# Performance work log

Hardware: AMD Instinct MI355X
Metric: run time of the kernel (lower is better)

Reference implementation:

```python
import jax, jax.numpy as jnp
import numpy as np

N_WAY = 5
NKPTS = 17
EMBED = 512
N_SUPPORT = 25  # 5-way 5-shot
N_QUERY = 65536


def setup_inputs() -> dict:
    key = jax.random.key(0)
    ks = jax.random.split(key, 12)
    def lin(k, fan_in, fan_out):
        return jax.random.normal(k, (fan_in, fan_out), jnp.float32) / np.float32(np.sqrt(fan_in))
    return {
        'support_features': jax.random.normal(ks[0], (1, N_SUPPORT, EMBED), jnp.float32),
        'support_keypoints': jax.random.uniform(ks[1], (N_SUPPORT, NKPTS, 2), jnp.float32),
        'query_features': jax.random.normal(ks[2], (N_QUERY, EMBED), jnp.float32),
        'image_coords': jax.random.uniform(ks[3], (N_QUERY, 2), jnp.float32) * 512.0,
        'W1': lin(ks[4], EMBED, EMBED), 'b1': jnp.zeros((EMBED,), jnp.float32),
        'W2': lin(ks[5], EMBED, EMBED), 'b2': jnp.zeros((EMBED,), jnp.float32),
        'Wo1': lin(ks[6], EMBED, EMBED // 2), 'bo1': jnp.zeros((EMBED // 2,), jnp.float32),
        'Wo2': lin(ks[7], EMBED // 2, 2), 'bo2': jnp.zeros((2,), jnp.float32),
        'Wc1': lin(ks[8], EMBED, EMBED // 2), 'bc1': jnp.zeros((EMBED // 2,), jnp.float32),
        'Wc2': lin(ks[9], EMBED // 2, 1), 'bc2': jnp.zeros((1,), jnp.float32),
        'temperature': jnp.float32(1.0),
    }


def reference(support_features, support_keypoints, query_features, image_coords,
              W1, b1, W2, b2, Wo1, bo1, Wo2, bo2, Wc1, bc1, Wc2, bc2, temperature):
    eps = 1e-8
    nkpts = support_keypoints.shape[1]
    n_query = query_features.shape[0]
    D = query_features.shape[-1]

    # --- compute_prototypes (batch_size == 1; per-kpt prototype identical by construction) ---
    sf = support_features.reshape(-1, D)                      # [Ns, D]
    h = jnp.maximum(sf @ W1 + b1, 0.0) @ W2 + b2              # prototype_net MLP
    n_per = h.shape[0] // N_WAY
    proto_way = h.reshape(N_WAY, n_per, D).mean(axis=1)       # [n_way, D]
    prototypes = jnp.broadcast_to(proto_way[:, None, :], (N_WAY, nkpts, D))

    # --- compute_distances: 1 - cosine_sim, scaled by temperature ---
    qn = jnp.linalg.norm(query_features, axis=-1)             # [Nq]
    pn = jnp.linalg.norm(proto_way, axis=-1)                  # [n_way]
    sim = (query_features @ proto_way.T) / jnp.maximum(qn[:, None] * pn[None, :], eps)
    dist_way = (1.0 - sim) / temperature                      # [Nq, n_way]
    distances = jnp.broadcast_to(dist_way[:, :, None], (n_query, N_WAY, nkpts))

    # --- predict_keypoints ---
    # avg over kpts is a no-op (identical per kpt); argmin over ways
    class_predictions = jnp.argmin(dist_way, axis=1)          # [Nq] int
    # softmax over a single scalar == 1.0, so keypoints == offset broadcast over kpts
    offset = jnp.maximum(query_features @ Wo1 + bo1, 0.0) @ Wo2 + bo2   # [Nq, 2]
    conf = jax.nn.sigmoid(jnp.maximum(query_features @ Wc1 + bc1, 0.0) @ Wc2 + bc2)  # [Nq, 1]
    keypoints = jnp.broadcast_to(offset[:, None, :], (n_query, nkpts, 2))
    keypoints = jax.nn.sigmoid(keypoints) * image_coords[:, None, :]    # image_coords provided
    confidence = jnp.broadcast_to(conf, (n_query, nkpts))

    return keypoints, confidence, distances, class_predictions, prototypes
```

## Files before the change

kernel.cpp:

```cpp
#include <hip/hip_runtime.h>
#include <hip/hip_bf16.h>

#define NQ 65536
#define DIM 512
#define HID 256
#define NWAY 5
#define NKPTS 17

typedef short bf16x8 __attribute__((ext_vector_type(8)));
typedef float f32x4 __attribute__((ext_vector_type(4)));
typedef _Float16 half8 __attribute__((ext_vector_type(8)));

static __device__ __forceinline__ unsigned short f2bf(float f) {
    unsigned int x = __float_as_uint(f);
    unsigned int r = (x + 0x7fffu + ((x >> 16) & 1u)) >> 16;
    return (unsigned short)r;
}

static __device__ __forceinline__ void async16(void* l, const void* g) {
    __builtin_amdgcn_global_load_lds(
        (const __attribute__((address_space(1))) unsigned int*)g,
        (__attribute__((address_space(3))) unsigned int*)l, 16, 0, 0);
}

__global__ __launch_bounds__(256) void k_sup(const float* __restrict__ sf,
                                             const float* __restrict__ W1, const float* __restrict__ b1,
                                             float* __restrict__ ws_h1) {
    __shared__ float sfl[512];
    __shared__ float red[4][64];
    int bx = blockIdx.x;
    int s = bx >> 3, cb = bx & 7;
    int t = threadIdx.x;
    if (t < 128) ((float4*)sfl)[t] = ((const float4*)(sf + s * DIM))[t];
    __syncthreads();
    int c = cb * 64 + (t & 63);
    int qd = t >> 6;
    const float* Wp = W1 + (size_t)qd * 128 * DIM + c;
    float acc = 0.0f;
    #pragma unroll 4
    for (int kk = 0; kk < 128; kk++)
        acc += sfl[qd * 128 + kk] * Wp[(size_t)kk * DIM];
    red[qd][t & 63] = acc;
    __syncthreads();
    if (t < 64) {
        float h = red[0][t] + red[1][t] + red[2][t] + red[3][t] + b1[cb * 64 + t];
        ws_h1[s * DIM + cb * 64 + t] = fmaxf(h, 0.0f);
    }
}

__global__ __launch_bounds__(256) void k_mid2(const float* __restrict__ ws_h1,
                                              const float* __restrict__ W2, const float* __restrict__ b2,
                                              const float* __restrict__ Wo1, const float* __restrict__ Wc1,
                                              float* __restrict__ ws_proto, unsigned short* __restrict__ wb) {
    int bx = blockIdx.x;
    int t = threadIdx.x;
    if (bx < 40) {
        __shared__ float ml[512];
        __shared__ float red[4][64];
        int w = bx >> 3, cb = bx & 7;
        for (int i = t; i < 512; i += 256) {
            float sum = 0.0f;
            #pragma unroll
            for (int s5 = 0; s5 < 5; s5++) sum += ws_h1[(w * 5 + s5) * DIM + i];
            ml[i] = sum * 0.2f;
        }
        __syncthreads();
        int c = cb * 64 + (t & 63);
        int qd = t >> 6;
        const float* Wp = W2 + (size_t)qd * 128 * DIM + c;
        float acc = 0.0f;
        #pragma unroll 4
        for (int kk = 0; kk < 128; kk++)
            acc += ml[qd * 128 + kk] * Wp[(size_t)kk * DIM];
        red[qd][t & 63] = acc;
        __syncthreads();
        if (t < 64)
            ws_proto[w * DIM + cb * 64 + t] =
                red[0][t] + red[1][t] + red[2][t] + red[3][t] + b2[cb * 64 + t];
    } else {
        __shared__ unsigned short T[64][72];
        int tb = bx - 40;
        const float* src = (tb < 32) ? Wo1 : Wc1;
        int cofs = (tb < 32) ? 0 : 256;
        int tt = tb & 31;
        int kt = tt >> 2;
        int ct = tt & 3;
        int i = t >> 2;
        int qd = t & 3;
        const float* rp = src + (size_t)(kt * 64 + i) * HID + ct * 64 + qd * 16;
        #pragma unroll
        for (int v = 0; v < 4; v++) {
            float4 x = *(const float4*)(rp + v * 4);
            T[qd * 16 + v * 4 + 0][i] = f2bf(x.x);
            T[qd * 16 + v * 4 + 1][i] = f2bf(x.y);
            T[qd * 16 + v * 4 + 2][i] = f2bf(x.z);
            T[qd * 16 + v * 4 + 3][i] = f2bf(x.w);
        }
        __syncthreads();
        int j = t >> 2;
        int part = t & 3;
        uint4 o0 = *(const uint4*)&T[j][part * 16];
        uint4 o1 = *(const uint4*)&T[j][part * 16 + 8];
        unsigned short* dst = wb + (size_t)(cofs + ct * 64 + j) * DIM + kt * 64 + part * 16;
        *(uint4*)dst = o0;
        *(uint4*)(dst + 8) = o1;
    }
}

__global__ __launch_bounds__(512) void k_fused3(const float* __restrict__ qf,
                                                const unsigned short* __restrict__ wb,
                                                const float* __restrict__ ws_proto,
                                                const float* __restrict__ temp_p,
                                                const float* __restrict__ bo1, const float* __restrict__ Wo2,
                                                const float* __restrict__ bo2,
                                                const float* __restrict__ bc1, const float* __restrict__ Wc2,
                                                const float* __restrict__ bc2,
                                                const float* __restrict__ ic,
                                                float* __restrict__ out_kp, float* __restrict__ out_conf,
                                                float* __restrict__ out_dist, float* __restrict__ out_class,
                                                float* __restrict__ out_proto) {
    __shared__ __align__(16) char smem[127520];
    char* Abase = smem;
    char* Bbase = smem + 16384;
    float* s_proto = (float*)(smem + 114688);
    float* dlds = (float*)(smem + 124928);
    float* pn_lds = (float*)(smem + 127488);
    _Float16* hl = (_Float16*)smem;
    float* redf = (float*)(smem + 67584);

    int mb = blockIdx.x;
    int t = threadIdx.x;
    int wv = t >> 6, lane = t & 63;
    int wr = wv >> 2, wc = wv & 3;
    int r = lane & 15, hq = lane >> 4;

    for (int i = t; i < NWAY * DIM; i += 512) s_proto[i] = ws_proto[i];
    if (mb < NWAY * NKPTS && t < 128) {
        f32x4 v = *(const f32x4*)(ws_proto + (mb / NKPTS) * DIM + t * 4);
        *(f32x4*)(out_proto + (size_t)mb * DIM + t * 4) = v;
    }
    float invt = 1.0f / temp_p[0];
    __syncthreads();

    if (wv < NWAY) {
        f32x4 a = *(const f32x4*)(s_proto + wv * DIM + lane * 8);
        f32x4 b = *(const f32x4*)(s_proto + wv * DIM + lane * 8 + 4);
        float ss = a[0]*a[0] + a[1]*a[1] + a[2]*a[2] + a[3]*a[3]
                 + b[0]*b[0] + b[1]*b[1] + b[2]*b[2] + b[3]*b[3];
        #pragma unroll
        for (int off = 32; off > 0; off >>= 1) ss += __shfl_xor(ss, off, 64);
        if (lane == 0) pn_lds[wv] = sqrtf(ss);
    }

    int am = t >> 2, akc = t & 3;
    const float* Ag = qf + ((size_t)mb * 128 + am) * DIM + akc * 8;
    int awoff = am * 64 + ((akc ^ (am & 3)) * 16);
    int srow = lane >> 2;
    int sg = (lane & 3) ^ (srow & 3);
    const unsigned short* Bg = wb + ((size_t)wv * 64 + srow) * DIM + sg * 8;

    f32x4 acc[4][8];
    #pragma unroll
    for (int i2 = 0; i2 < 4; i2++)
        #pragma unroll
        for (int j2 = 0; j2 < 8; j2++) { f32x4 z = {0.0f, 0.0f, 0.0f, 0.0f}; acc[i2][j2] = z; }
    float ds[NWAY] = {0, 0, 0, 0, 0};
    float qq = 0.0f;

    float4 aW0 = *(const float4*)(Ag);
    float4 aW1 = *(const float4*)(Ag + 4);
    float4 aN0 = *(const float4*)(Ag + 32);
    float4 aN1 = *(const float4*)(Ag + 36);
    #pragma unroll
    for (int i = 0; i < 4; i++)
        async16(Bbase + (wv * 4 + i) * 1024, Bg + (size_t)i * 16 * DIM);
    #pragma unroll
    for (int i = 0; i < 4; i++)
        async16(Bbase + 32768 + (wv * 4 + i) * 1024, Bg + (size_t)i * 16 * DIM + 32);

    {
        unsigned int p0 = f2bf(aW0.x) | ((unsigned int)f2bf(aW0.y) << 16);
        unsigned int p1 = f2bf(aW0.z) | ((unsigned int)f2bf(aW0.w) << 16);
        unsigned int p2 = f2bf(aW1.x) | ((unsigned int)f2bf(aW1.y) << 16);
        unsigned int p3 = f2bf(aW1.z) | ((unsigned int)f2bf(aW1.w) << 16);
        *(uint4*)(Abase + awoff) = make_uint4(p0, p1, p2, p3);
        float av[8] = {aW0.x, aW0.y, aW0.z, aW0.w, aW1.x, aW1.y, aW1.z, aW1.w};
        int kb = akc * 8;
        #pragma unroll
        for (int w = 0; w < NWAY; w++) {
            f32x4 pv0 = *(const f32x4*)(s_proto + w * DIM + kb);
            f32x4 pv1 = *(const f32x4*)(s_proto + w * DIM + kb + 4);
            ds[w] += av[0] * pv0[0] + av[1] * pv0[1] + av[2] * pv0[2] + av[3] * pv0[3]
                   + av[4] * pv1[0] + av[5] * pv1[1] + av[6] * pv1[2] + av[7] * pv1[3];
        }
        #pragma unroll
        for (int j = 0; j < 8; j++) qq += av[j] * av[j];
    }
    aW0 = aN0; aW1 = aN1;

    asm volatile("s_waitcnt lgkmcnt(0) vmcnt(4)" ::: "memory");
    __builtin_amdgcn_s_barrier();
    __builtin_amdgcn_sched_barrier(0);

    #pragma unroll 2
    for (int it = 0; it < 16; it++) {
        int apar = it & 1;
        int bpar = it % 3;
        float4 aL0, aL1;
        if (it < 14) {
            int ko = (it + 2) * 32;
            aL0 = *(const float4*)(Ag + ko);
            aL1 = *(const float4*)(Ag + ko + 4);
            int bp2 = (it + 2) % 3;
            #pragma unroll
            for (int i = 0; i < 4; i++)
                async16(Bbase + bp2 * 32768 + (wv * 4 + i) * 1024,
                        Bg + (size_t)i * 16 * DIM + ko);
        }
        if (it < 15) {
            unsigned int p0 = f2bf(aW0.x) | ((unsigned int)f2bf(aW0.y) << 16);
            unsigned int p1 = f2bf(aW0.z) | ((unsigned int)f2bf(aW0.w) << 16);
            unsigned int p2 = f2bf(aW1.x) | ((unsigned int)f2bf(aW1.y) << 16);
            unsigned int p3 = f2bf(aW1.z) | ((unsigned int)f2bf(aW1.w) << 16);
            *(uint4*)(Abase + (apar ^ 1) * 8192 + awoff) = make_uint4(p0, p1, p2, p3);
            float av[8] = {aW0.x, aW0.y, aW0.z, aW0.w, aW1.x, aW1.y, aW1.z, aW1.w};
            int kb = (it + 1) * 32 + akc * 8;
            #pragma unroll
            for (int w = 0; w < NWAY; w++) {
                f32x4 pv0 = *(const f32x4*)(s_proto + w * DIM + kb);
                f32x4 pv1 = *(const f32x4*)(s_proto + w * DIM + kb + 4);
                ds[w] += av[0] * pv0[0] + av[1] * pv0[1] + av[2] * pv0[2] + av[3] * pv0[3]
                       + av[4] * pv1[0] + av[5] * pv1[1] + av[6] * pv1[2] + av[7] * pv1[3];
            }
            #pragma unroll
            for (int j = 0; j < 8; j++) qq += av[j] * av[j];
        }
        const unsigned short* Ap = (const unsigned short*)(Abase + apar * 8192);
        const unsigned short* Bp = (const unsigned short*)(Bbase + bpar * 32768);
        int sl = (hq ^ (r & 3)) * 8;
        bf16x8 af[4], bfr[8];
        #pragma unroll
        for (int mt = 0; mt < 4; mt++)
            af[mt] = *(const bf16x8*)(Ap + (wr * 64 + mt * 16 + r) * 32 + sl);
        #pragma unroll
        for (int nt = 0; nt < 8; nt++)
            bfr[nt] = *(const bf16x8*)(Bp + (wc * 128 + nt * 16 + r) * 32 + sl);
        #pragma unroll
        for (int mt = 0; mt < 4; mt++)
            #pragma unroll
            for (int nt = 0; nt < 8; nt++)
                acc[mt][nt] = __builtin_amdgcn_mfma_f32_16x16x32_bf16(af[mt], bfr[nt], acc[mt][nt], 0, 0, 0);
        if (it < 15) {
            if (it < 14) { asm volatile("s_waitcnt lgkmcnt(0) vmcnt(6)" ::: "memory"); }
            else         { asm volatile("s_waitcnt lgkmcnt(0) vmcnt(0)" ::: "memory"); }
            __builtin_amdgcn_s_barrier();
            __builtin_amdgcn_sched_barrier(0);
        }
        if (it < 14) { aW0 = aL0; aW1 = aL1; }
    }
    __syncthreads();

    if (wc < 2) {
        #pragma unroll
        for (int nt = 0; nt < 8; nt++) {
            int cl = wc * 128 + nt * 16 + r;
            float bv = bo1[cl];
            #pragma unroll
            for (int mt = 0; mt < 4; mt++)
                #pragma unroll
                for (int rg = 0; rg < 4; rg++) {
                    int ml = wr * 64 + mt * 16 + hq * 4 + rg;
                    hl[ml * 264 + cl] = (_Float16)fmaxf(acc[mt][nt][rg] + bv, 0.0f);
                }
        }
    }
    __syncthreads();

    #pragma unroll
    for (int off = 1; off <= 2; off <<= 1) {
        #pragma unroll
        for (int w = 0; w < NWAY; w++) ds[w] += __shfl_xor(ds[w], off, 64);
        qq += __shfl_xor(qq, off, 64);
    }
    if (akc == 0) {
        float qn = sqrtf(qq);
        float mv = 1e30f; int ami = 0;
        #pragma unroll
        for (int w = 0; w < NWAY; w++) {
            float den = fmaxf(qn * pn_lds[w], 1e-8f);
            float d = (1.0f - ds[w] / den) * invt;
            dlds[am * 5 + w] = d;
            if (d < mv) { mv = d; ami = w; }
        }
        out_class[mb * 128 + am] = (float)ami;
    }
    {
        int q = t & 127, qt = t >> 7;
        float ox = 0.0f, oy = 0.0f;
        #pragma unroll 2
        for (int j0 = 0; j0 < 64; j0 += 8) {
            half8 hv = *(const half8*)(hl + q * 264 + qt * 64 + j0);
            #pragma unroll
            for (int j = 0; j < 8; j++) {
                float2 w2 = *(const float2*)(Wo2 + (qt * 64 + j0 + j) * 2);
                float hf = (float)hv[j];
                ox += hf * w2.x;
                oy += hf * w2.y;
            }
        }
        redf[(qt * 128 + q) * 2] = ox;
        redf[(qt * 128 + q) * 2 + 1] = oy;
    }
    __syncthreads();

    if (t < 128) {
        float sx = bo2[0], sy = bo2[1];
        #pragma unroll
        for (int k2 = 0; k2 < 4; k2++) {
            sx += redf[(k2 * 128 + t) * 2];
            sy += redf[(k2 * 128 + t) * 2 + 1];
        }
        size_t Q = (size_t)mb * 128 + t;
        float2 icv = *(const float2*)(ic + Q * 2);
        float gx = icv.x / (1.0f + __expf(-sx));
        float gy = icv.y / (1.0f + __expf(-sy));
        float2 g2 = make_float2(gx, gy);
        float2* dst = (float2*)(out_kp + Q * 34);
        #pragma unroll
        for (int k2 = 0; k2 < 17; k2++) dst[k2] = g2;
    }
    if (wc >= 2) {
        #pragma unroll
        for (int nt = 0; nt < 8; nt++) {
            int cl = (wc - 2) * 128 + nt * 16 + r;
            float bv = bc1[cl];
            #pragma unroll
            for (int mt = 0; mt < 4; mt++)
                #pragma unroll
                for (int rg = 0; rg < 4; rg++) {
                    int ml = wr * 64 + mt * 16 + hq * 4 + rg;
                    hl[ml * 264 + cl] = (_Float16)fmaxf(acc[mt][nt][rg] + bv, 0.0f);
                }
        }
    }
    for (int i = t; i < 128 * NWAY * NKPTS; i += 512) {
        int q2 = i / (NWAY * NKPTS);
        int rem = i - q2 * (NWAY * NKPTS);
        out_dist[(size_t)(mb * 128 + q2) * (NWAY * NKPTS) + rem] = dlds[q2 * 5 + rem / NKPTS];
    }
    __syncthreads();

    {
        int q = t & 127, qt = t >> 7;
        float cs = 0.0f;
        #pragma unroll 2
        for (int j0 = 0; j0 < 64; j0 += 8) {
            half8 hv = *(const half8*)(hl + q * 264 + qt * 64 + j0);
            #pragma unroll
            for (int j = 0; j < 8; j++)
                cs += (float)hv[j] * Wc2[qt * 64 + j0 + j];
        }
        redf[qt * 128 + q] = cs;
    }
    __syncthreads();
    if (t < 128) {
        float s = bc2[0] + redf[t] + redf[128 + t] + redf[256 + t] + redf[384 + t];
        float sg2 = 1.0f / (1.0f + __expf(-s));
        size_t Q = (size_t)mb * 128 + t;
        float* dst = out_conf + Q * 17;
        #pragma unroll
        for (int k2 = 0; k2 < 17; k2++) dst[k2] = sg2;
    }
}

extern "C" void kernel_launch(void* const* d_in, const int* in_sizes, int n_in,
                              void* d_out, int out_size, void* d_ws, size_t ws_size,
                              hipStream_t stream) {
    const float* sf = (const float*)d_in[0];
    const float* qf = (const float*)d_in[2];
    const float* ic = (const float*)d_in[3];
    const float* W1 = (const float*)d_in[4];
    const float* b1 = (const float*)d_in[5];
    const float* W2 = (const float*)d_in[6];
    const float* b2 = (const float*)d_in[7];
    const float* Wo1 = (const float*)d_in[8];
    const float* bo1 = (const float*)d_in[9];
    const float* Wo2 = (const float*)d_in[10];
    const float* bo2 = (const float*)d_in[11];
    const float* Wc1 = (const float*)d_in[12];
    const float* bc1 = (const float*)d_in[13];
    const float* Wc2 = (const float*)d_in[14];
    const float* bc2 = (const float*)d_in[15];
    const float* temp = (const float*)d_in[16];

    float* out = (float*)d_out;
    float* out_kp = out;
    float* out_conf = out + 2228224;
    float* out_dist = out + 3342336;
    float* out_class = out + 8912896;
    float* out_proto = out + 8978432;

    char* ws = (char*)d_ws;
    float* ws_h1 = (float*)ws;
    float* ws_proto = (float*)(ws + 51200);
    unsigned short* ws_wb = (unsigned short*)(ws + 65536);

    hipLaunchKernelGGL(k_sup, dim3(200), dim3(256), 0, stream, sf, W1, b1, ws_h1);
    hipLaunchKernelGGL(k_mid2, dim3(104), dim3(256), 0, stream, ws_h1, W2, b2, Wo1, Wc1, ws_proto, ws_wb);
    hipLaunchKernelGGL(k_fused3, dim3(512), dim3(512), 0, stream, qf, ws_wb, ws_proto, temp,
                       bo1, Wo2, bo2, bc1, Wc2, bc2, ic, out_kp, out_conf,
                       out_dist, out_class, out_proto);
}
```

Before: 318.2 us.

## Split fused query kernel into separate distance kernel and N-split GEMM kernel

```diff
diff --git a/kernel.cpp b/kernel.cpp
--- a/kernel.cpp
+++ b/kernel.cpp
@@ -107,195 +107,208 @@
     }
 }
 
-__global__ __launch_bounds__(512) void k_fused3(const float* __restrict__ qf,
-                                                const unsigned short* __restrict__ wb,
-                                                const float* __restrict__ ws_proto,
-                                                const float* __restrict__ temp_p,
-                                                const float* __restrict__ bo1, const float* __restrict__ Wo2,
-                                                const float* __restrict__ bo2,
-                                                const float* __restrict__ bc1, const float* __restrict__ Wc2,
-                                                const float* __restrict__ bc2,
-                                                const float* __restrict__ ic,
-                                                float* __restrict__ out_kp, float* __restrict__ out_conf,
-                                                float* __restrict__ out_dist, float* __restrict__ out_class,
-                                                float* __restrict__ out_proto) {
-    __shared__ __align__(16) char smem[127520];
-    char* Abase = smem;
-    char* Bbase = smem + 16384;
-    float* s_proto = (float*)(smem + 114688);
-    float* dlds = (float*)(smem + 124928);
-    float* pn_lds = (float*)(smem + 127488);
+__global__ __launch_bounds__(256) void k_dist(const float* __restrict__ qf,
+                                              const float* __restrict__ ws_proto,
+                                              const float* __restrict__ temp_p,
+                                              float* __restrict__ out_dist, float* __restrict__ out_class,
+                                              float* __restrict__ out_proto) {
+    __shared__ float pn_lds[8];
+    __shared__ float dlds[64 * NWAY];
+    int bx = blockIdx.x, t = threadIdx.x;
+    int wv = t >> 6, lane = t & 63;
+
+    if (bx < NWAY * NKPTS && t < 128) {
+        f32x4 v = *(const f32x4*)(ws_proto + (bx / NKPTS) * DIM + t * 4);
+        *(f32x4*)(out_proto + (size_t)bx * DIM + t * 4) = v;
+    }
+    for (int w = wv; w < NWAY; w += 4) {
+        f32x4 a = *(const f32x4*)(ws_proto + w * DIM + lane * 8);
+        f32x4 b = *(const f32x4*)(ws_proto + w * DIM + lane * 8 + 4);
+        float ss = a[0]*a[0] + a[1]*a[1] + a[2]*a[2] + a[3]*a[3]
+                 + b[0]*b[0] + b[1]*b[1] + b[2]*b[2] + b[3]*b[3];
+        #pragma unroll
+        for (int off = 32; off > 0; off >>= 1) ss += __shfl_xor(ss, off, 64);
+        if (lane == 0) pn_lds[w] = sqrtf(ss);
+    }
+    float invt = 1.0f / temp_p[0];
+    __syncthreads();
+
+    int q = bx * 64 + wv * 16 + (lane & 15);
+    int kq = (lane >> 4) * 128;
+    const float* qp = qf + (size_t)q * DIM + kq;
+    const float* pp = ws_proto + kq;
+
+    float ds[NWAY] = {0, 0, 0, 0, 0};
+    float qq = 0.0f;
+    #pragma unroll 4
+    for (int c = 0; c < 16; c++) {
+        f32x4 v0 = *(const f32x4*)(qp + c * 8);
+        f32x4 v1 = *(const f32x4*)(qp + c * 8 + 4);
+        qq += v0[0]*v0[0] + v0[1]*v0[1] + v0[2]*v0[2] + v0[3]*v0[3]
+            + v1[0]*v1[0] + v1[1]*v1[1] + v1[2]*v1[2] + v1[3]*v1[3];
+        #pragma unroll
+        for (int w = 0; w < NWAY; w++) {
+            f32x4 p0 = *(const f32x4*)(pp + w * DIM + c * 8);
+            f32x4 p1 = *(const f32x4*)(pp + w * DIM + c * 8 + 4);
+            ds[w] += v0[0]*p0[0] + v0[1]*p0[1] + v0[2]*p0[2] + v0[3]*p0[3]
+                   + v1[0]*p1[0] + v1[1]*p1[1] + v1[2]*p1[2] + v1[3]*p1[3];
+        }
+    }
+    #pragma unroll
+    for (int off = 16; off <= 32; off <<= 1) {
+        #pragma unroll
+        for (int w = 0; w < NWAY; w++) ds[w] += __shfl_xor(ds[w], off, 64);
+        qq += __shfl_xor(qq, off, 64);
+    }
+    if (lane < 16) {
+        float qn = sqrtf(qq);
+        float mv = 1e30f; int ami = 0;
+        #pragma unroll
+        for (int w = 0; w < NWAY; w++) {
+            float den = fmaxf(qn * pn_lds[w], 1e-8f);
+            float d = (1.0f - ds[w] / den) * invt;
+            dlds[(wv * 16 + lane) * NWAY + w] = d;
+            if (d < mv) { mv = d; ami = w; }
+        }
+        out_class[q] = (float)ami;
+    }
+    __syncthreads();
+    int Q0 = bx * 64;
+    for (int i = t; i < 64 * NWAY * NKPTS; i += 256) {
+        int q2 = i / (NWAY * NKPTS);
+        int rem = i - q2 * (NWAY * NKPTS);
+        out_dist[(size_t)(Q0 + q2) * (NWAY * NKPTS) + rem] = dlds[q2 * NWAY + rem / NKPTS];
+    }
+}
+
+__global__ __launch_bounds__(256, 3) void k_gemm(const float* __restrict__ qf,
+                                                 const unsigned short* __restrict__ wb,
+                                                 const float* __restrict__ bo1, const float* __restrict__ Wo2,
+                                                 const float* __restrict__ bo2,
+                                                 const float* __restrict__ bc1, const float* __restrict__ Wc2,
+                                                 const float* __restrict__ bc2,
+                                                 const float* __restrict__ ic,
+                                                 float* __restrict__ out_kp, float* __restrict__ out_conf) {
+    __shared__ __align__(16) char smem[40960];
+    char* Ab = smem;
+    char* Bb = smem + 8192;
     _Float16* hl = (_Float16*)smem;
-    float* redf = (float*)(smem + 67584);
-
-    int mb = blockIdx.x;
+    float* redf = (float*)(smem + 33792);
+
+    int bx = blockIdx.x;
+    int mb = bx & 1023, nb = bx >> 10;
     int t = threadIdx.x;
     int wv = t >> 6, lane = t & 63;
-    int wr = wv >> 2, wc = wv & 3;
     int r = lane & 15, hq = lane >> 4;
 
-    for (int i = t; i < NWAY * DIM; i += 512) s_proto[i] = ws_proto[i];
-    if (mb < NWAY * NKPTS && t < 128) {
-        f32x4 v = *(const f32x4*)(ws_proto + (mb / NKPTS) * DIM + t * 4);
-        *(f32x4*)(out_proto + (size_t)mb * DIM + t * 4) = v;
-    }
-    float invt = 1.0f / temp_p[0];
-    __syncthreads();
-
-    if (wv < NWAY) {
-        f32x4 a = *(const f32x4*)(s_proto + wv * DIM + lane * 8);
-        f32x4 b = *(const f32x4*)(s_proto + wv * DIM + lane * 8 + 4);
-        float ss = a[0]*a[0] + a[1]*a[1] + a[2]*a[2] + a[3]*a[3]
-                 + b[0]*b[0] + b[1]*b[1] + b[2]*b[2] + b[3]*b[3];
-        #pragma unroll
-        for (int off = 32; off > 0; off >>= 1) ss += __shfl_xor(ss, off, 64);
-        if (lane == 0) pn_lds[wv] = sqrtf(ss);
-    }
-
     int am = t >> 2, akc = t & 3;
-    const float* Ag = qf + ((size_t)mb * 128 + am) * DIM + akc * 8;
-    int awoff = am * 64 + ((akc ^ (am & 3)) * 16);
+    const float* Ag = qf + ((size_t)mb * 64 + am) * DIM + akc * 8;
+    int awoff = am * 64 + ((akc ^ (am & 3) ^ ((am >> 2) & 1)) << 4);
+
     int srow = lane >> 2;
-    int sg = (lane & 3) ^ (srow & 3);
-    const unsigned short* Bg = wb + ((size_t)wv * 64 + srow) * DIM + sg * 8;
-
-    f32x4 acc[4][8];
+    int sg = (lane & 3) ^ (srow & 3) ^ ((srow >> 2) & 1);
+    const unsigned short* Bg = wb + (size_t)(nb * 256 + wv * 64 + srow) * DIM + sg * 8;
+
+    f32x4 acc[4][4];
     #pragma unroll
     for (int i2 = 0; i2 < 4; i2++)
         #pragma unroll
-        for (int j2 = 0; j2 < 8; j2++) { f32x4 z = {0.0f, 0.0f, 0.0f, 0.0f}; acc[i2][j2] = z; }
-    float ds[NWAY] = {0, 0, 0, 0, 0};
-    float qq = 0.0f;
+        for (int j2 = 0; j2 < 4; j2++) { f32x4 z = {0.0f, 0.0f, 0.0f, 0.0f}; acc[i2][j2] = z; }
 
     float4 aW0 = *(const float4*)(Ag);
     float4 aW1 = *(const float4*)(Ag + 4);
+    #pragma unroll
+    for (int i = 0; i < 4; i++)
+        async16(Bb + wv * 4096 + i * 1024, Bg + (size_t)i * 16 * DIM);
     float4 aN0 = *(const float4*)(Ag + 32);
     float4 aN1 = *(const float4*)(Ag + 36);
-    #pragma unroll
-    for (int i = 0; i < 4; i++)
-        async16(Bbase + (wv * 4 + i) * 1024, Bg + (size_t)i * 16 * DIM);
-    #pragma unroll
-    for (int i = 0; i < 4; i++)
-        async16(Bbase + 32768 + (wv * 4 + i) * 1024, Bg + (size_t)i * 16 * DIM + 32);
-
     {
         unsigned int p0 = f2bf(aW0.x) | ((unsigned int)f2bf(aW0.y) << 16);
         unsigned int p1 = f2bf(aW0.z) | ((unsigned int)f2bf(aW0.w) << 16);
         unsigned int p2 = f2bf(aW1.x) | ((unsigned int)f2bf(aW1.y) << 16);
         unsigned int p3 = f2bf(aW1.z) | ((unsigned int)f2bf(aW1.w) << 16);
-        *(uint4*)(Abase + awoff) = make_uint4(p0, p1, p2, p3);
-        float av[8] = {aW0.x, aW0.y, aW0.z, aW0.w, aW1.x, aW1.y, aW1.z, aW1.w};
-        int kb = akc * 8;
-        #pragma unroll
-        for (int w = 0; w < NWAY; w++) {
-            f32x4 pv0 = *(const f32x4*)(s_proto + w * DIM + kb);
-            f32x4 pv1 = *(const f32x4*)(s_proto + w * DIM + kb + 4);
-            ds[w] += av[0] * pv0[0] + av[1] * pv0[1] + av[2] * pv0[2] + av[3] * pv0[3]
-                   + av[4] * pv1[0] + av[5] * pv1[1] + av[6] * pv1[2] + av[7] * pv1[3];
-        }
-        #pragma unroll
-        for (int j = 0; j < 8; j++) qq += av[j] * av[j];
+        *(uint4*)(Ab + awoff) = make_uint4(p0, p1, p2, p3);
     }
     aW0 = aN0; aW1 = aN1;
-
-    asm volatile("s_waitcnt lgkmcnt(0) vmcnt(4)" ::: "memory");
+    asm volatile("s_waitcnt lgkmcnt(0) vmcnt(2)" ::: "memory");
     __builtin_amdgcn_s_barrier();
     __builtin_amdgcn_sched_barrier(0);
 
-    #pragma unroll 2
-    for (int it = 0; it < 16; it++) {
-        int apar = it & 1;
-        int bpar = it % 3;
+    int slot8 = (hq ^ (r & 3) ^ ((r >> 2) & 1)) * 8;
+
+    for (int it = 0; it < 15; it++) {
+        int par = it & 1;
+        #pragma unroll
+        for (int i = 0; i < 4; i++)
+            async16(Bb + (par ^ 1) * 16384 + wv * 4096 + i * 1024,
+                    Bg + (size_t)i * 16 * DIM + (it + 1) * 32);
         float4 aL0, aL1;
         if (it < 14) {
-            int ko = (it + 2) * 32;
-            aL0 = *(const float4*)(Ag + ko);
-            aL1 = *(const float4*)(Ag + ko + 4);
-            int bp2 = (it + 2) % 3;
-            #pragma unroll
-            for (int i = 0; i < 4; i++)
-                async16(Bbase + bp2 * 32768 + (wv * 4 + i) * 1024,
-                        Bg + (size_t)i * 16 * DIM + ko);
-        }
-        if (it < 15) {
+            aL0 = *(const float4*)(Ag + (it + 2) * 32);
+            aL1 = *(const float4*)(Ag + (it + 2) * 32 + 4);
+        }
+        {
             unsigned int p0 = f2bf(aW0.x) | ((unsigned int)f2bf(aW0.y) << 16);
             unsigned int p1 = f2bf(aW0.z) | ((unsigned int)f2bf(aW0.w) << 16);
             unsigned int p2 = f2bf(aW1.x) | ((unsigned int)f2bf(aW1.y) << 16);
             unsigned int p3 = f2bf(aW1.z) | ((unsigned int)f2bf(aW1.w) << 16);
-            *(uint4*)(Abase + (apar ^ 1) * 8192 + awoff) = make_uint4(p0, p1, p2, p3);
-            float av[8] = {aW0.x, aW0.y, aW0.z, aW0.w, aW1.x, aW1.y, aW1.z, aW1.w};
-            int kb = (it + 1) * 32 + akc * 8;
-            #pragma unroll
-            for (int w = 0; w < NWAY; w++) {
-                f32x4 pv0 = *(const f32x4*)(s_proto + w * DIM + kb);
-                f32x4 pv1 = *(const f32x4*)(s_proto + w * DIM + kb + 4);
-                ds[w] += av[0] * pv0[0] + av[1] * pv0[1] + av[2] * pv0[2] + av[3] * pv0[3]
-                       + av[4] * pv1[0] + av[5] * pv1[1] + av[6] * pv1[2] + av[7] * pv1[3];
+            *(uint4*)(Ab + (par ^ 1) * 4096 + awoff) = make_uint4(p0, p1, p2, p3);
+        }
+        const unsigned short* Ap = (const unsigned short*)(Ab + par * 4096);
+        const unsigned short* Bp = (const unsigned short*)(Bb + par * 16384);
+        bf16x8 af[4], bfr[4];
+        #pragma unroll
+        for (int mt = 0; mt < 4; mt++)
+            af[mt] = *(const bf16x8*)(Ap + (mt * 16 + r) * 32 + slot8);
+        #pragma unroll
+        for (int nt = 0; nt < 4; nt++)
+            bfr[nt] = *(const bf16x8*)(Bp + (wv * 64 + nt * 16 + r) * 32 + slot8);
+        #pragma unroll
+        for (int mt = 0; mt < 4; mt++)
+            #pragma unroll
+            for (int nt = 0; nt < 4; nt++)
+                acc[mt][nt] = __builtin_amdgcn_mfma_f32_16x16x32_bf16(af[mt], bfr[nt], acc[mt][nt], 0, 0, 0);
+        if (it < 14) { asm volatile("s_waitcnt lgkmcnt(0) vmcnt(2)" ::: "memory"); }
+        else         { asm volatile("s_waitcnt lgkmcnt(0) vmcnt(0)" ::: "memory"); }
+        __builtin_amdgcn_s_barrier();
+        __builtin_amdgcn_sched_barrier(0);
+        if (it < 14) { aW0 = aL0; aW1 = aL1; }
+    }
+    {
+        const unsigned short* Ap = (const unsigned short*)(Ab + 4096);
+        const unsigned short* Bp = (const unsigned short*)(Bb + 16384);
+        bf16x8 af[4], bfr[4];
+        #pragma unroll
+        for (int mt = 0; mt < 4; mt++)
+            af[mt] = *(const bf16x8*)(Ap + (mt * 16 + r) * 32 + slot8);
+        #pragma unroll
+        for (int nt = 0; nt < 4; nt++)
+            bfr[nt] = *(const bf16x8*)(Bp + (wv * 64 + nt * 16 + r) * 32 + slot8);
+        #pragma unroll
+        for (int mt = 0; mt < 4; mt++)
+            #pragma unroll
+            for (int nt = 0; nt < 4; nt++)
+                acc[mt][nt] = __builtin_amdgcn_mfma_f32_16x16x32_bf16(af[mt], bfr[nt], acc[mt][nt], 0, 0, 0);
+    }
+    __syncthreads();
+
+    const float* bias = nb ? bc1 : bo1;
+    #pragma unroll
+    for (int nt = 0; nt < 4; nt++) {
+        int cl = wv * 64 + nt * 16 + r;
+        float bv = bias[cl];
+        #pragma unroll
+        for (int mt = 0; mt < 4; mt++)
+            #pragma unroll
+            for (int rg = 0; rg < 4; rg++) {
+                int ml = mt * 16 + hq * 4 + rg;
+                hl[ml * 264 + cl] = (_Float16)fmaxf(acc[mt][nt][rg] + bv, 0.0f);
             }
-            #pragma unroll
-            for (int j = 0; j < 8; j++) qq += av[j] * av[j];
-        }
-        const unsigned short* Ap = (const unsigned short*)(Abase + apar * 8192);
-        const unsigned short* Bp = (const unsigned short*)(Bbase + bpar * 32768);
-        int sl = (hq ^ (r & 3)) * 8;
-        bf16x8 af[4], bfr[8];
-        #pragma unroll
-        for (int mt = 0; mt < 4; mt++)
-            af[mt] = *(const bf16x8*)(Ap + (wr * 64 + mt * 16 + r) * 32 + sl);
-        #pragma unroll
-        for (int nt = 0; nt < 8; nt++)
-            bfr[nt] = *(const bf16x8*)(Bp + (wc * 128 + nt * 16 + r) * 32 + sl);
-        #pragma unroll
-        for (int mt = 0; mt < 4; mt++)
-            #pragma unroll
-            for (int nt = 0; nt < 8; nt++)
-                acc[mt][nt] = __builtin_amdgcn_mfma_f32_16x16x32_bf16(af[mt], bfr[nt], acc[mt][nt], 0, 0, 0);
-        if (it < 15) {
-            if (it < 14) { asm volatile("s_waitcnt lgkmcnt(0) vmcnt(6)" ::: "memory"); }
-            else         { asm volatile("s_waitcnt lgkmcnt(0) vmcnt(0)" ::: "memory"); }
-            __builtin_amdgcn_s_barrier();
-            __builtin_amdgcn_sched_barrier(0);
-        }
-        if (it < 14) { aW0 = aL0; aW1 = aL1; }
-    }
-    __syncthreads();
-
-    if (wc < 2) {
-        #pragma unroll
-        for (int nt = 0; nt < 8; nt++) {
-            int cl = wc * 128 + nt * 16 + r;
-            float bv = bo1[cl];
-            #pragma unroll
-            for (int mt = 0; mt < 4; mt++)
-                #pragma unroll
-                for (int rg = 0; rg < 4; rg++) {
-                    int ml = wr * 64 + mt * 16 + hq * 4 + rg;
-                    hl[ml * 264 + cl] = (_Float16)fmaxf(acc[mt][nt][rg] + bv, 0.0f);
-                }
-        }
-    }
-    __syncthreads();
-
-    #pragma unroll
-    for (int off = 1; off <= 2; off <<= 1) {
-        #pragma unroll
-        for (int w = 0; w < NWAY; w++) ds[w] += __shfl_xor(ds[w], off, 64);
-        qq += __shfl_xor(qq, off, 64);
-    }
-    if (akc == 0) {
-        float qn = sqrtf(qq);
-        float mv = 1e30f; int ami = 0;
-        #pragma unroll
-        for (int w = 0; w < NWAY; w++) {
-            float den = fmaxf(qn * pn_lds[w], 1e-8f);
-            float d = (1.0f - ds[w] / den) * invt;
-            dlds[am * 5 + w] = d;
-            if (d < mv) { mv = d; ami = w; }
-        }
-        out_class[mb * 128 + am] = (float)ami;
-    }
-    {
-        int q = t & 127, qt = t >> 7;
+    }
+    __syncthreads();
+
+    int q = t & 63, qt = t >> 6;
+    if (nb == 0) {
         float ox = 0.0f, oy = 0.0f;
         #pragma unroll 2
         for (int j0 = 0; j0 < 64; j0 += 8) {
@@ -308,50 +321,26 @@
                 oy += hf * w2.y;
             }
         }
-        redf[(qt * 128 + q) * 2] = ox;
-        redf[(qt * 128 + q) * 2 + 1] = oy;
-    }
-    __syncthreads();
-
-    if (t < 128) {
-        float sx = bo2[0], sy = bo2[1];
-        #pragma unroll
-        for (int k2 = 0; k2 < 4; k2++) {
-            sx += redf[(k2 * 128 + t) * 2];
-            sy += redf[(k2 * 128 + t) * 2 + 1];
-        }
-        size_t Q = (size_t)mb * 128 + t;
-        float2 icv = *(const float2*)(ic + Q * 2);
-        float gx = icv.x / (1.0f + __expf(-sx));
-        float gy = icv.y / (1.0f + __expf(-sy));
-        float2 g2 = make_float2(gx, gy);
-        float2* dst = (float2*)(out_kp + Q * 34);
-        #pragma unroll
-        for (int k2 = 0; k2 < 17; k2++) dst[k2] = g2;
-    }
-    if (wc >= 2) {
-        #pragma unroll
-        for (int nt = 0; nt < 8; nt++) {
-            int cl = (wc - 2) * 128 + nt * 16 + r;
-            float bv = bc1[cl];
-            #pragma unroll
-            for (int mt = 0; mt < 4; mt++)
-                #pragma unroll
-                for (int rg = 0; rg < 4; rg++) {
-                    int ml = wr * 64 + mt * 16 + hq * 4 + rg;
-                    hl[ml * 264 + cl] = (_Float16)fmaxf(acc[mt][nt][rg] + bv, 0.0f);
-                }
-        }
-    }
-    for (int i = t; i < 128 * NWAY * NKPTS; i += 512) {
-        int q2 = i / (NWAY * NKPTS);
-        int rem = i - q2 * (NWAY * NKPTS);
-        out_dist[(size_t)(mb * 128 + q2) * (NWAY * NKPTS) + rem] = dlds[q2 * 5 + rem / NKPTS];
-    }
-    __syncthreads();
-
-    {
-        int q = t & 127, qt = t >> 7;
+        redf[(qt * 64 + q) * 2] = ox;
+        redf[(qt * 64 + q) * 2 + 1] = oy;
+        __syncthreads();
+        if (t < 64) {
+            float sx = bo2[0], sy = bo2[1];
+            #pragma unroll
+            for (int k2 = 0; k2 < 4; k2++) {
+                sx += redf[(k2 * 64 + t) * 2];
+                sy += redf[(k2 * 64 + t) * 2 + 1];
+            }
+            size_t Q = (size_t)mb * 64 + t;
+            float2 icv = *(const float2*)(ic + Q * 2);
+            float gx = icv.x / (1.0f + __expf(-sx));
+            float gy = icv.y / (1.0f + __expf(-sy));
+            float2 g2 = make_float2(gx, gy);
+            float2* dst = (float2*)(out_kp + Q * 34);
+            #pragma unroll
+            for (int k2 = 0; k2 < 17; k2++) dst[k2] = g2;
+        }
+    } else {
         float cs = 0.0f;
         #pragma unroll 2
         for (int j0 = 0; j0 < 64; j0 += 8) {
@@ -360,16 +349,16 @@
             for (int j = 0; j < 8; j++)
                 cs += (float)hv[j] * Wc2[qt * 64 + j0 + j];
         }
-        redf[qt * 128 + q] = cs;
-    }
-    __syncthreads();
-    if (t < 128) {
-        float s = bc2[0] + redf[t] + redf[128 + t] + redf[256 + t] + redf[384 + t];
-        float sg2 = 1.0f / (1.0f + __expf(-s));
-        size_t Q = (size_t)mb * 128 + t;
-        float* dst = out_conf + Q * 17;
-        #pragma unroll
-        for (int k2 = 0; k2 < 17; k2++) dst[k2] = sg2;
+        redf[qt * 64 + q] = cs;
+        __syncthreads();
+        if (t < 64) {
+            float s = bc2[0] + redf[t] + redf[64 + t] + redf[128 + t] + redf[192 + t];
+            float sg2 = 1.0f / (1.0f + __expf(-s));
+            size_t Q = (size_t)mb * 64 + t;
+            float* dst = out_conf + Q * 17;
+            #pragma unroll
+            for (int k2 = 0; k2 < 17; k2++) dst[k2] = sg2;
+        }
     }
 }
 
@@ -407,7 +396,8 @@
 
     hipLaunchKernelGGL(k_sup, dim3(200), dim3(256), 0, stream, sf, W1, b1, ws_h1);
     hipLaunchKernelGGL(k_mid2, dim3(104), dim3(256), 0, stream, ws_h1, W2, b2, Wo1, Wc1, ws_proto, ws_wb);
-    hipLaunchKernelGGL(k_fused3, dim3(512), dim3(512), 0, stream, qf, ws_wb, ws_proto, temp,
-                       bo1, Wo2, bo2, bc1, Wc2, bc2, ic, out_kp, out_conf,
+    hipLaunchKernelGGL(k_dist, dim3(1024), dim3(256), 0, stream, qf, ws_proto, temp,
                        out_dist, out_class, out_proto);
-}
+    hipLaunchKernelGGL(k_gemm, dim3(2048), dim3(256), 0, stream, qf, ws_wb,
+                       bo1, Wo2, bo2, bc1, Wc2, bc2, ic, out_kp, out_conf);
+}
```

New measurement: 349.3 us. +9.8%, slower.
